# Performance work log

Hardware: AMD Instinct MI355X
Metric: run time of the kernel (lower is better)

The kernel has to match this reference:

```python
import jax, jax.numpy as jnp
import numpy as np

N_NODES = 50000
N_EDGES = 800000
IN_FEATS = 256
NUM_HEADS = 8
OUT_FEATS = 32
NEG_SLOPE = 0.2


def setup_inputs() -> dict:
    key = jax.random.key(0)
    ks = jax.random.split(key, 10)
    feat = jax.random.normal(ks[0], (N_NODES, IN_FEATS), dtype=jnp.float32)
    edge_emb = jax.random.normal(ks[1], (N_EDGES, NUM_HEADS), dtype=jnp.float32)
    src = jax.random.randint(ks[2], (N_EDGES,), 0, N_NODES, dtype=jnp.int32)
    dst = jax.random.randint(ks[3], (N_EDGES,), 0, N_NODES, dtype=jnp.int32)
    # learned params (xavier-style scale)
    W_src = jax.random.normal(ks[4], (IN_FEATS, NUM_HEADS * OUT_FEATS), dtype=jnp.float32) * 0.05
    W_e = jax.random.normal(ks[5], (NUM_HEADS, NUM_HEADS * OUT_FEATS), dtype=jnp.float32) * 0.3
    attn_l = jax.random.normal(ks[6], (NUM_HEADS, OUT_FEATS), dtype=jnp.float32) * 0.2
    attn_r = jax.random.normal(ks[7], (NUM_HEADS, OUT_FEATS), dtype=jnp.float32) * 0.2
    attn_e = jax.random.normal(ks[8], (NUM_HEADS, OUT_FEATS), dtype=jnp.float32) * 0.2
    bias = jnp.zeros((NUM_HEADS * OUT_FEATS,), dtype=jnp.float32)
    return {"feat": feat, "edge_emb": edge_emb, "src": src, "dst": dst,
            "W_src": W_src, "W_e": W_e, "attn_l": attn_l, "attn_r": attn_r,
            "attn_e": attn_e, "bias": bias}


def reference(feat, edge_emb, src, dst, W_src, W_e, attn_l, attn_r, attn_e, bias):
    N = feat.shape[0]
    H, D = attn_l.shape
    # node projections (share_weights=True -> fc_dst is fc_src)
    h = (feat @ W_src).reshape(N, H, D)            # (N, H, D)
    ef = (edge_emb @ W_e).reshape(-1, H, D)        # (E, H, D)
    # per-head attention scalars
    el = jnp.einsum("nhd,hd->nh", h, attn_l)      # (N, H)
    er = jnp.einsum("nhd,hd->nh", h, attn_r)      # (N, H)
    ee = jnp.einsum("ehd,hd->eh", ef, attn_e)     # (E, H)
    logits = jax.nn.leaky_relu(el[src] + er[dst] + ee, NEG_SLOPE)  # (E, H)
    # edge softmax over incoming edges of each dst node (numerically stable)
    m = jax.ops.segment_max(logits, dst, num_segments=N)
    m = jnp.where(jnp.isfinite(m), m, 0.0)
    p = jnp.exp(logits - m[dst])
    s = jax.ops.segment_sum(p, dst, num_segments=N)
    alpha = p / (s[dst] + 1e-9)                    # (E, H)
    # weighted message aggregation
    out = jax.ops.segment_sum(alpha[:, :, None] * h[src], dst, num_segments=N)  # (N, H, D)
    out = out + bias.reshape(1, H, D)
    return out
```

## Files before the change

### kernel.cpp

```cpp
#include <hip/hip_runtime.h>

#define H 8
#define D 32
#define HD 256
#define NEG_SLOPE 0.2f
#define SCB 1024

typedef __attribute__((ext_vector_type(8))) short bf8;
typedef __attribute__((ext_vector_type(4))) float f4;

__device__ __forceinline__ unsigned short f2b(float x) {
    unsigned u = __float_as_uint(x);
    unsigned r = (u + 0x7fffu + ((u >> 16) & 1u)) >> 16;
    return (unsigned short)r;
}

__global__ __launch_bounds__(256) void k_prep(
        const float* __restrict__ W, unsigned short* __restrict__ Wtb,
        const float* __restrict__ W_e, const float* __restrict__ attn_e,
        float* __restrict__ M, const int* __restrict__ dst, int* __restrict__ cnt,
        int* __restrict__ ord, int E, int bh) {
    const int b = blockIdx.x, t = threadIdx.x;
    if (b < HD) {
        Wtb[b * HD + t] = f2b(W[t * HD + b]);
    } else if (b < HD + bh) {
        int e = (b - HD) * 256 + t;
        if (e < E) ord[e] = atomicAdd(&cnt[dst[e]], 1);
    } else {
        if (t < 64) {
            int k = t >> 3, hh = t & 7;
            float acc = 0.f;
            for (int d = 0; d < D; ++d)
                acc = fmaf(W_e[k * HD + hh * D + d], attn_e[hh * D + d], acc);
            M[k * 8 + hh] = acc;
        }
    }
}

__global__ __launch_bounds__(1024) void k_scan1(const int* __restrict__ cnt,
                                                int* __restrict__ offs,
                                                int* __restrict__ btot, int N) {
    __shared__ int wtot[16], wbase[16];
    const int t = threadIdx.x, wid = t >> 6, lane = t & 63;
    int i = blockIdx.x * SCB + t;
    int v = (i < N) ? cnt[i] : 0;
    int x = v;
#pragma unroll
    for (int off = 1; off < 64; off <<= 1) {
        int y = __shfl_up(x, off, 64);
        if (lane >= off) x += y;
    }
    if (lane == 63) wtot[wid] = x;
    __syncthreads();
    if (t < 16) {
        int w = wtot[t], xs = w;
#pragma unroll
        for (int off = 1; off < 16; off <<= 1) {
            int y = __shfl_up(xs, off, 64);
            if (t >= off) xs += y;
        }
        wbase[t] = xs - w;
        if (t == 15) btot[blockIdx.x] = xs;
    }
    __syncthreads();
    if (i < N) offs[i] = wbase[wid] + (x - v);
}

__global__ __launch_bounds__(1024) void k_scan3(int* __restrict__ offs,
                                                const int* __restrict__ btot,
                                                int N, int E, int nb) {
    __shared__ int bb;
    const int t = threadIdx.x;
    if (t < 64) {
        int vv = (t < nb) ? btot[t] : 0;
        int x = vv;
#pragma unroll
        for (int off = 1; off < 64; off <<= 1) {
            int y = __shfl_up(x, off, 64);
            if (t >= off) x += y;
        }
        if (t == blockIdx.x) bb = x - vv;
    }
    __syncthreads();
    const int i = blockIdx.x * SCB + t;
    if (i < N) offs[i] += bb;
    if (i == 0) offs[N] = E;
}

__global__ __launch_bounds__(512) void k_fuse(
        const float* __restrict__ feat, const unsigned short* __restrict__ Wtb,
        const float* __restrict__ attn_l, const float* __restrict__ attn_r,
        unsigned short* __restrict__ hb, float* __restrict__ el,
        float* __restrict__ er, int N, int bg,
        const int* __restrict__ src, const int* __restrict__ dst,
        const int* __restrict__ offs, const int* __restrict__ ord,
        uint2* __restrict__ pair, int E) {
    const int t = threadIdx.x;
    if (blockIdx.x >= bg) {
        const int base = (blockIdx.x - bg) * 2048;
        const int end = min(base + 2048, E);
        for (int e = base + t; e < end; e += 512) {
            int p = offs[dst[e]] + ord[e];
            pair[p] = make_uint2((unsigned)src[e], (unsigned)e);
        }
        return;
    }
    __shared__ unsigned short lwt[128 * HD];
    const int l = t & 63, wv = t >> 6;
    const int row0 = (blockIdx.x * 8 + wv) * 16;
    const bool act = row0 < N;
    const int m = l & 15, q = l >> 4;

    bf8 afr[8];
    if (act) {
        const float* arow = feat + (size_t)(row0 + m) * HD + q * 8;
#pragma unroll
        for (int kc = 0; kc < 8; ++kc) {
            const float4 f0 = *(const float4*)(arow + kc * 32);
            const float4 f1 = *(const float4*)(arow + kc * 32 + 4);
            bf8 a;
            a[0] = (short)f2b(f0.x); a[1] = (short)f2b(f0.y);
            a[2] = (short)f2b(f0.z); a[3] = (short)f2b(f0.w);
            a[4] = (short)f2b(f1.x); a[5] = (short)f2b(f1.y);
            a[6] = (short)f2b(f1.z); a[7] = (short)f2b(f1.w);
            afr[kc] = a;
        }
    }

    f4 acc[16];
#pragma unroll
    for (int nt = 0; nt < 16; ++nt) acc[nt] = (f4){0.f, 0.f, 0.f, 0.f};

    const uint4* wt4 = (const uint4*)Wtb;
    uint4* l4 = (uint4*)lwt;
#pragma unroll
    for (int half = 0; half < 2; ++half) {
        if (half) __syncthreads();
#pragma unroll
        for (int i = 0; i < 8; ++i) {
            const int u = i * 512 + t;
            l4[u ^ ((u >> 5) & 7)] = wt4[half * 4096 + u];
        }
        __syncthreads();
        if (act) {
#pragma unroll
            for (int ntl = 0; ntl < 8; ++ntl) {
                const int nt = half * 8 + ntl;
                const int lc = ntl * 16 + m;
                const unsigned short* bp = lwt + lc * HD;
                const int sw = (lc & 7) * 8;
#pragma unroll
                for (int kc = 0; kc < 8; ++kc) {
                    const bf8 b = *(const bf8*)(bp + ((q * 8 + kc * 32) ^ sw));
                    acc[nt] = __builtin_amdgcn_mfma_f32_16x16x32_bf16(
                                  afr[kc], b, acc[nt], 0, 0, 0);
                }
            }
        }
    }
    if (!act) return;

#pragma unroll
    for (int h = 0; h < H; ++h) {
        float elp[4] = {0.f, 0.f, 0.f, 0.f};
        float erp[4] = {0.f, 0.f, 0.f, 0.f};
#pragma unroll
        for (int s = 0; s < 2; ++s) {
            const int nt = h * 2 + s;
            const int c = nt * 16 + m;
            const float alc = attn_l[c];
            const float arc = attn_r[c];
#pragma unroll
            for (int reg = 0; reg < 4; ++reg) {
                const float v = acc[nt][reg];
                hb[(size_t)(row0 + q * 4 + reg) * HD + c] = f2b(v);
                elp[reg] = fmaf(v, alc, elp[reg]);
                erp[reg] = fmaf(v, arc, erp[reg]);
            }
        }
#pragma unroll
        for (int reg = 0; reg < 4; ++reg) {
#pragma unroll
            for (int off = 1; off < 16; off <<= 1) {
                elp[reg] += __shfl_xor(elp[reg], off, 16);
                erp[reg] += __shfl_xor(erp[reg], off, 16);
            }
        }
        if (m == 0) {
#pragma unroll
            for (int reg = 0; reg < 4; ++reg) {
                el[(row0 + q * 4 + reg) * H + h] = elp[reg];
                er[(row0 + q * 4 + reg) * H + h] = erp[reg];
            }
        }
    }
}

__global__ __launch_bounds__(256) void k_node(
        const int* __restrict__ offs, const uint2* __restrict__ pair,
        const float* __restrict__ edge_emb, const float* __restrict__ el,
        const float* __restrict__ er, const float* __restrict__ M,
        const unsigned short* __restrict__ hb, const float* __restrict__ bias,
        float* __restrict__ out, int N) {
    const int t = threadIdx.x;
    const int lane = t & 63;
    const int v = blockIdx.x * 4 + (t >> 6);
    if (v >= N) return;
    const int hh = lane & 7;
    const int sl = lane & 31;
    const int half = lane >> 5;
    const int cb = sl * 8;
    const int hq = sl >> 2;
    const int s0 = offs[v];
    const int deg = offs[v + 1] - s0;

    float Mreg[8];
#pragma unroll
    for (int k = 0; k < 8; ++k) Mreg[k] = M[k * 8 + hh];
    const float erv = er[(size_t)v * 8 + hh];
    const unsigned short* hbc = hb + cb;

    float a[8];
#pragma unroll
    for (int i = 0; i < 8; ++i) a[i] = 0.f;
    float psum = 0.f;

    for (int j0 = 0; j0 < deg; j0 += 64) {
        const int nj = min(64, deg - j0);
        uint2 prl = make_uint2(0u, 0u);
        if (lane < nj) prl = pair[s0 + j0 + lane];

        float pv[8];
#pragma unroll
        for (int s = 0; s < 8; ++s) {
            pv[s] = 0.f;
            if (s * 8 < nj) {
                const int j = s * 8 + (lane >> 3);
                const unsigned sx = __shfl(prl.x, j, 64);
                const unsigned ex = __shfl(prl.y, j, 64);
                const float eev = edge_emb[(size_t)ex * 8 + hh];
                float lg = el[(size_t)sx * 8 + hh] + erv;
#pragma unroll
                for (int k = 0; k < 8; ++k)
                    lg = fmaf(__shfl(eev, k, 8), Mreg[k], lg);
                lg = (lg >= 0.f) ? lg : NEG_SLOPE * lg;
                if (j < nj) { pv[s] = __expf(lg); psum += pv[s]; }
            }
        }

#pragma unroll
        for (int s = 0; s < 8; ++s) {
            if (s * 8 >= nj) break;
#pragma unroll
            for (int u = 0; u < 4; ++u) {
                if (s * 8 + 2 * u >= nj) break;
                const int jj = 2 * u + half;
                const unsigned sx = __shfl(prl.x, s * 8 + jj, 64);
                const float pj = __shfl(pv[s], jj * 8 + hq, 64);
                const uint4 w = *(const uint4*)(hbc + (size_t)sx * HD);
                a[0] = fmaf(pj, __uint_as_float(w.x << 16), a[0]);
                a[1] = fmaf(pj, __uint_as_float(w.x & 0xffff0000u), a[1]);
                a[2] = fmaf(pj, __uint_as_float(w.y << 16), a[2]);
                a[3] = fmaf(pj, __uint_as_float(w.y & 0xffff0000u), a[3]);
                a[4] = fmaf(pj, __uint_as_float(w.z << 16), a[4]);
                a[5] = fmaf(pj, __uint_as_float(w.z & 0xffff0000u), a[5]);
                a[6] = fmaf(pj, __uint_as_float(w.w << 16), a[6]);
                a[7] = fmaf(pj, __uint_as_float(w.w & 0xffff0000u), a[7]);
            }
        }
    }

#pragma unroll
    for (int i = 0; i < 8; ++i) a[i] += __shfl_xor(a[i], 32, 64);

    psum += __shfl_xor(psum, 8, 64);
    psum += __shfl_xor(psum, 16, 64);
    psum += __shfl_xor(psum, 32, 64);
    const float rs = 1.f / (__shfl(psum, hq, 8) + 1e-9f);
    if (half == 0) {
        const float4 b0 = *(const float4*)&bias[cb];
        const float4 b1 = *(const float4*)&bias[cb + 4];
        *(float4*)&out[(size_t)v * HD + cb] =
            make_float4(fmaf(a[0], rs, b0.x), fmaf(a[1], rs, b0.y),
                        fmaf(a[2], rs, b0.z), fmaf(a[3], rs, b0.w));
        *(float4*)&out[(size_t)v * HD + cb + 4] =
            make_float4(fmaf(a[4], rs, b1.x), fmaf(a[5], rs, b1.y),
                        fmaf(a[6], rs, b1.z), fmaf(a[7], rs, b1.w));
    }
}

extern "C" void kernel_launch(void* const* d_in, const int* in_sizes, int n_in,
                              void* d_out, int out_size, void* d_ws, size_t ws_size,
                              hipStream_t stream) {
    const float* feat     = (const float*)d_in[0];
    const float* edge_emb = (const float*)d_in[1];
    const int*   src      = (const int*)d_in[2];
    const int*   dst      = (const int*)d_in[3];
    const float* W_src    = (const float*)d_in[4];
    const float* W_e      = (const float*)d_in[5];
    const float* attn_l   = (const float*)d_in[6];
    const float* attn_r   = (const float*)d_in[7];
    const float* attn_e   = (const float*)d_in[8];
    const float* bias     = (const float*)d_in[9];
    float* out = (float*)d_out;

    const int N = in_sizes[0] / HD;
    const int E = in_sizes[2];

    char* ws = (char*)d_ws;
    unsigned short* hb = (unsigned short*)ws; ws += (size_t)N * HD * 2;
    uint2* pair = (uint2*)ws; ws += (size_t)E * 8;
    float* el   = (float*)ws; ws += (size_t)N * H * 4;
    float* er   = (float*)ws; ws += (size_t)N * H * 4;
    int*   cnt  = (int*)ws;   ws += (size_t)N * 4;
    int* offs   = (int*)ws; ws += (size_t)(N + 1) * 4;
    int* ord    = (int*)ws; ws += (size_t)E * 4;
    unsigned short* Wtb = (unsigned short*)ws; ws += (size_t)HD * HD * 2;
    int* btot  = (int*)ws; ws += 64 * 4;
    float* M   = (float*)ws; ws += 256;

    const int bh  = (E + 255) / 256;
    const int nsb = (N + SCB - 1) / SCB;
    const int bg  = ((N + 15) / 16 + 7) / 8;
    const int bs  = (E + 2047) / 2048;

    hipMemsetAsync(cnt, 0, (size_t)N * 4, stream);
    k_prep  <<<HD + bh + 1, 256, 0, stream>>>(W_src, Wtb, W_e, attn_e, M,
                                              dst, cnt, ord, E, bh);
    k_scan1 <<<nsb, SCB, 0, stream>>>(cnt, offs, btot, N);
    k_scan3 <<<nsb, SCB, 0, stream>>>(offs, btot, N, E, nsb);
    k_fuse  <<<bg + bs, 512, 0, stream>>>(feat, Wtb, attn_l, attn_r, hb, el, er,
                                          N, bg, src, dst, offs, ord, pair, E);
    k_node  <<<(N + 3) / 4, 256, 0, stream>>>(offs, pair, edge_emb, el, er, M,
                                              hb, bias, out, N);
}
```

Measured before the change: 296.6 us.

## Precompute edge logits in CSR order with atomic scatter, batch gathers in node kernel

The edge-logit computation (el[src] plus the edge_emb·M projection) moves out of the node kernel into a new per-edge kernel. That kernel scatters logits and source ids into CSR order using atomic cursors seeded from the scanned offsets. The degree histogram moves into the projection kernel, and the separate memset and ord array are dropped. The node kernel now reads contiguous precomputed logits and issues eight h-row gathers before accumulating, to raise memory-level parallelism. The cost is an extra E×8 float write and read plus one more launch, and edge order within a segment becomes nondeterministic.

```diff
diff --git a/kernel.cpp b/kernel.cpp
--- a/kernel.cpp
+++ b/kernel.cpp
@@ -15,18 +15,14 @@
     return (unsigned short)r;
 }
 
-__global__ __launch_bounds__(256) void k_prep(
+__global__ __launch_bounds__(256) void k0(
         const float* __restrict__ W, unsigned short* __restrict__ Wtb,
         const float* __restrict__ W_e, const float* __restrict__ attn_e,
-        float* __restrict__ M, const int* __restrict__ dst, int* __restrict__ cnt,
-        int* __restrict__ ord, int E, int bh) {
+        float* __restrict__ M, int* __restrict__ cnt, int N) {
     const int b = blockIdx.x, t = threadIdx.x;
     if (b < HD) {
         Wtb[b * HD + t] = f2b(W[t * HD + b]);
-    } else if (b < HD + bh) {
-        int e = (b - HD) * 256 + t;
-        if (e < E) ord[e] = atomicAdd(&cnt[dst[e]], 1);
-    } else {
+    } else if (b == HD) {
         if (t < 64) {
             int k = t >> 3, hh = t & 7;
             float acc = 0.f;
@@ -34,6 +30,9 @@
                 acc = fmaf(W_e[k * HD + hh * D + d], attn_e[hh * D + d], acc);
             M[k * 8 + hh] = acc;
         }
+    } else {
+        int i = (b - HD - 1) * 256 + t;
+        if (i < N) cnt[i] = 0;
     }
 }
 
@@ -68,6 +67,7 @@
 
 __global__ __launch_bounds__(1024) void k_scan3(int* __restrict__ offs,
                                                 const int* __restrict__ btot,
+                                                int* __restrict__ cur,
                                                 int N, int E, int nb) {
     __shared__ int bb;
     const int t = threadIdx.x;
@@ -83,7 +83,11 @@
     }
     __syncthreads();
     const int i = blockIdx.x * SCB + t;
-    if (i < N) offs[i] += bb;
+    if (i < N) {
+        const int o = offs[i] + bb;
+        offs[i] = o;
+        cur[i] = o;
+    }
     if (i == 0) offs[N] = E;
 }
 
@@ -92,17 +96,13 @@
         const float* __restrict__ attn_l, const float* __restrict__ attn_r,
         unsigned short* __restrict__ hb, float* __restrict__ el,
         float* __restrict__ er, int N, int bg,
-        const int* __restrict__ src, const int* __restrict__ dst,
-        const int* __restrict__ offs, const int* __restrict__ ord,
-        uint2* __restrict__ pair, int E) {
+        const int* __restrict__ dst, int* __restrict__ cnt, int E) {
     const int t = threadIdx.x;
     if (blockIdx.x >= bg) {
         const int base = (blockIdx.x - bg) * 2048;
         const int end = min(base + 2048, E);
-        for (int e = base + t; e < end; e += 512) {
-            int p = offs[dst[e]] + ord[e];
-            pair[p] = make_uint2((unsigned)src[e], (unsigned)e);
-        }
+        for (int e = base + t; e < end; e += 512)
+            atomicAdd(&cnt[dst[e]], 1);
         return;
     }
     __shared__ unsigned short lwt[128 * HD];
@@ -196,10 +196,50 @@
     }
 }
 
+__global__ __launch_bounds__(256) void k_edge(
+        const int* __restrict__ src, const int* __restrict__ dst,
+        const float* __restrict__ edge_emb, const float* __restrict__ el,
+        const float* __restrict__ Mg, int* __restrict__ cur,
+        int* __restrict__ src_csr, float* __restrict__ lgcsr, int E) {
+    const int t = threadIdx.x;
+    float Mreg[8][8];
+#pragma unroll
+    for (int k = 0; k < 8; ++k) {
+        const float4 m0 = *(const float4*)(Mg + k * 8);
+        const float4 m1 = *(const float4*)(Mg + k * 8 + 4);
+        Mreg[k][0] = m0.x; Mreg[k][1] = m0.y; Mreg[k][2] = m0.z; Mreg[k][3] = m0.w;
+        Mreg[k][4] = m1.x; Mreg[k][5] = m1.y; Mreg[k][6] = m1.z; Mreg[k][7] = m1.w;
+    }
+    const int base = blockIdx.x * 1024;
+    const int end = min(base + 1024, E);
+    for (int e = base + t; e < end; e += 256) {
+        const int se = src[e], de = dst[e];
+        const float4 e0 = ((const float4*)edge_emb)[e * 2];
+        const float4 e1 = ((const float4*)edge_emb)[e * 2 + 1];
+        const float4 l0 = ((const float4*)el)[se * 2];
+        const float4 l1 = ((const float4*)el)[se * 2 + 1];
+        const float ee[8] = {e0.x, e0.y, e0.z, e0.w, e1.x, e1.y, e1.z, e1.w};
+        const float ela[8] = {l0.x, l0.y, l0.z, l0.w, l1.x, l1.y, l1.z, l1.w};
+        float lg[8];
+#pragma unroll
+        for (int hh = 0; hh < 8; ++hh) {
+            float x = ela[hh];
+#pragma unroll
+            for (int k = 0; k < 8; ++k)
+                x = fmaf(ee[k], Mreg[k][hh], x);
+            lg[hh] = x;
+        }
+        const int p = atomicAdd(&cur[de], 1);
+        src_csr[p] = se;
+        float4* o = (float4*)&lgcsr[(size_t)p * 8];
+        o[0] = make_float4(lg[0], lg[1], lg[2], lg[3]);
+        o[1] = make_float4(lg[4], lg[5], lg[6], lg[7]);
+    }
+}
+
 __global__ __launch_bounds__(256) void k_node(
-        const int* __restrict__ offs, const uint2* __restrict__ pair,
-        const float* __restrict__ edge_emb, const float* __restrict__ el,
-        const float* __restrict__ er, const float* __restrict__ M,
+        const int* __restrict__ offs, const int* __restrict__ src_csr,
+        const float* __restrict__ lgcsr, const float* __restrict__ er,
         const unsigned short* __restrict__ hb, const float* __restrict__ bias,
         float* __restrict__ out, int N) {
     const int t = threadIdx.x;
@@ -214,9 +254,6 @@
     const int s0 = offs[v];
     const int deg = offs[v + 1] - s0;
 
-    float Mreg[8];
-#pragma unroll
-    for (int k = 0; k < 8; ++k) Mreg[k] = M[k * 8 + hh];
     const float erv = er[(size_t)v * 8 + hh];
     const unsigned short* hbc = hb + cb;
 
@@ -227,8 +264,9 @@
 
     for (int j0 = 0; j0 < deg; j0 += 64) {
         const int nj = min(64, deg - j0);
-        uint2 prl = make_uint2(0u, 0u);
-        if (lane < nj) prl = pair[s0 + j0 + lane];
+        int srcl = 0;
+        if (lane < nj) srcl = src_csr[s0 + j0 + lane];
+        const float* lgb = lgcsr + (size_t)(s0 + j0) * 8;
 
         float pv[8];
 #pragma unroll
@@ -236,28 +274,33 @@
             pv[s] = 0.f;
             if (s * 8 < nj) {
                 const int j = s * 8 + (lane >> 3);
-                const unsigned sx = __shfl(prl.x, j, 64);
-                const unsigned ex = __shfl(prl.y, j, 64);
-                const float eev = edge_emb[(size_t)ex * 8 + hh];
-                float lg = el[(size_t)sx * 8 + hh] + erv;
-#pragma unroll
-                for (int k = 0; k < 8; ++k)
-                    lg = fmaf(__shfl(eev, k, 8), Mreg[k], lg);
-                lg = (lg >= 0.f) ? lg : NEG_SLOPE * lg;
-                if (j < nj) { pv[s] = __expf(lg); psum += pv[s]; }
-            }
-        }
-
-#pragma unroll
-        for (int s = 0; s < 8; ++s) {
-            if (s * 8 >= nj) break;
-#pragma unroll
-            for (int u = 0; u < 4; ++u) {
-                if (s * 8 + 2 * u >= nj) break;
-                const int jj = 2 * u + half;
-                const unsigned sx = __shfl(prl.x, s * 8 + jj, 64);
+                if (j < nj) {
+                    float x = lgb[s * 64 + lane] + erv;
+                    x = (x >= 0.f) ? x : NEG_SLOPE * x;
+                    pv[s] = __expf(x);
+                    psum += pv[s];
+                }
+            }
+        }
+
+#pragma unroll
+        for (int g = 0; g < 4; ++g) {
+            if (g * 16 >= nj) break;
+            int sx8[8];
+            uint4 w8[8];
+#pragma unroll
+            for (int i = 0; i < 8; ++i) {
+                const int s = 2 * g + (i >> 2);
+                const int jj = 2 * (i & 3) + half;
+                sx8[i] = __shfl(srcl, s * 8 + jj, 64);
+                w8[i] = *(const uint4*)(hbc + (size_t)sx8[i] * HD);
+            }
+#pragma unroll
+            for (int i = 0; i < 8; ++i) {
+                const int s = 2 * g + (i >> 2);
+                const int jj = 2 * (i & 3) + half;
                 const float pj = __shfl(pv[s], jj * 8 + hq, 64);
-                const uint4 w = *(const uint4*)(hbc + (size_t)sx * HD);
+                const uint4 w = w8[i];
                 a[0] = fmaf(pj, __uint_as_float(w.x << 16), a[0]);
                 a[1] = fmaf(pj, __uint_as_float(w.x & 0xffff0000u), a[1]);
                 a[2] = fmaf(pj, __uint_as_float(w.y << 16), a[2]);
@@ -309,28 +352,29 @@
 
     char* ws = (char*)d_ws;
     unsigned short* hb = (unsigned short*)ws; ws += (size_t)N * HD * 2;
-    uint2* pair = (uint2*)ws; ws += (size_t)E * 8;
+    float* lgcsr = (float*)ws; ws += (size_t)E * H * 4;
+    int* src_csr = (int*)ws; ws += (size_t)E * 4;
     float* el   = (float*)ws; ws += (size_t)N * H * 4;
     float* er   = (float*)ws; ws += (size_t)N * H * 4;
     int*   cnt  = (int*)ws;   ws += (size_t)N * 4;
+    int*   cur  = cnt;
     int* offs   = (int*)ws; ws += (size_t)(N + 1) * 4;
-    int* ord    = (int*)ws; ws += (size_t)E * 4;
     unsigned short* Wtb = (unsigned short*)ws; ws += (size_t)HD * HD * 2;
     int* btot  = (int*)ws; ws += 64 * 4;
     float* M   = (float*)ws; ws += 256;
 
-    const int bh  = (E + 255) / 256;
+    const int nz  = (N + 255) / 256;
     const int nsb = (N + SCB - 1) / SCB;
     const int bg  = ((N + 15) / 16 + 7) / 8;
-    const int bs  = (E + 2047) / 2048;
-
-    hipMemsetAsync(cnt, 0, (size_t)N * 4, stream);
-    k_prep  <<<HD + bh + 1, 256, 0, stream>>>(W_src, Wtb, W_e, attn_e, M,
-                                              dst, cnt, ord, E, bh);
+    const int bhist = (E + 2047) / 2048;
+
+    k0      <<<HD + 1 + nz, 256, 0, stream>>>(W_src, Wtb, W_e, attn_e, M, cnt, N);
+    k_fuse  <<<bg + bhist, 512, 0, stream>>>(feat, Wtb, attn_l, attn_r, hb, el, er,
+                                             N, bg, dst, cnt, E);
     k_scan1 <<<nsb, SCB, 0, stream>>>(cnt, offs, btot, N);
-    k_scan3 <<<nsb, SCB, 0, stream>>>(offs, btot, N, E, nsb);
-    k_fuse  <<<bg + bs, 512, 0, stream>>>(feat, Wtb, attn_l, attn_r, hb, el, er,
-                                          N, bg, src, dst, offs, ord, pair, E);
-    k_node  <<<(N + 3) / 4, 256, 0, stream>>>(offs, pair, edge_emb, el, er, M,
+    k_scan3 <<<nsb, SCB, 0, stream>>>(offs, btot, cur, N, E, nsb);
+    k_edge  <<<(E + 1023) / 1024, 256, 0, stream>>>(src, dst, edge_emb, el, M,
+                                                    cur, src_csr, lgcsr, E);
+    k_node  <<<(N + 3) / 4, 256, 0, stream>>>(offs, src_csr, lgcsr, er,
                                               hb, bias, out, N);
 }
```

New measurement: 301.6 us. Within noise of the previous version (+1.7%).
